# Kernel optimization log

Measured on AMD Instinct MI355X. Metric: run time of the kernel, lower is better.

Reference implementation:

```python
import jax, jax.numpy as jnp
import numpy as np

B, S, D, H, L, F = 1, 2048, 768, 12, 2, 3072
DH = D // H          # 64
W = 256              # one-sided sliding window (attention_window=512 total)
NC = S // W          # number of query chunks
VOCAB = 50265


def _ln(x, s, b, eps=1e-5):
    m = x.mean(-1, keepdims=True)
    v = ((x - m) ** 2).mean(-1, keepdims=True)
    return (x - m) / jnp.sqrt(v + eps) * s + b


def setup_inputs() -> dict:
    key = jax.random.key(0)
    ks = jax.random.split(key, 16)
    p = lambda k, sh: jax.random.normal(k, sh, jnp.float32) * 0.02
    return {
        "input_ids": jax.random.randint(ks[0], (B, S), 0, VOCAB),
        "attention_mask": jnp.ones((B, S), jnp.int32),
        "word_emb": p(ks[1], (VOCAB, D)),
        "pos_emb": p(ks[2], (S + 2, D)),          # roberta-style pos ids start at 2
        "type_emb": p(ks[3], (1, D)),
        "emb_ln_s": jnp.ones((D,), jnp.float32),
        "emb_ln_b": jnp.zeros((D,), jnp.float32),
        "Wqkv": p(ks[4], (L, 3, D, D)),
        "bqkv": jnp.zeros((L, 3, D), jnp.float32),
        "Wo": p(ks[5], (L, D, D)),
        "bo": jnp.zeros((L, D), jnp.float32),
        "ln1_s": jnp.ones((L, D), jnp.float32),
        "ln1_b": jnp.zeros((L, D), jnp.float32),
        "W1": p(ks[6], (L, D, F)),
        "b1": jnp.zeros((L, F), jnp.float32),
        "W2": p(ks[7], (L, F, D)),
        "b2": jnp.zeros((L, D), jnp.float32),
        "ln2_s": jnp.ones((L, D), jnp.float32),
        "ln2_b": jnp.zeros((L, D), jnp.float32),
        "pool_W": p(ks[8], (D, D)),
        "pool_b": jnp.zeros((D,), jnp.float32),
    }


def reference(input_ids, attention_mask, word_emb, pos_emb, type_emb,
              emb_ln_s, emb_ln_b, Wqkv, bqkv, Wo, bo, ln1_s, ln1_b,
              W1, b1, W2, b2, ln2_s, ln2_b, pool_W, pool_b):
    # ---- embeddings (roberta/longformer style) ----
    pos_ids = jnp.cumsum(attention_mask, axis=1) * attention_mask + 1  # padding_idx=1
    x = word_emb[input_ids] + pos_emb[pos_ids] + type_emb[0]
    x = _ln(x, emb_ln_s, emb_ln_b)

    # ---- banded-attention index/mask precompute (int constants) ----
    idx = jnp.arange(NC)[:, None] * W + jnp.arange(3 * W)[None, :]      # [NC, 3W] into padded seq
    rel = (jnp.arange(3 * W)[None, :] - W) - jnp.arange(W)[:, None]     # key_pos - query_pos
    band = (rel >= -W) & (rel <= W)                                      # [W, 3W]
    kmask = jnp.pad(attention_mask, ((0, 0), (W, W)))[:, idx].astype(bool)  # [B, NC, 3W]
    valid = band[None, None] & kmask[:, :, None, :]                      # [B, NC, W, 3W]

    inv_sqrt_dh = 1.0 / np.sqrt(DH)
    for l in range(L):
        qkv = jnp.einsum('bsd,tde->tbse', x, Wqkv[l]) + bqkv[l][:, None, None, :]
        q, k, v = [t.reshape(B, S, H, DH).transpose(0, 2, 1, 3) for t in qkv]  # [B,H,S,DH]
        qc = q.reshape(B, H, NC, W, DH)
        kp = jnp.pad(k, ((0, 0), (0, 0), (W, W), (0, 0)))
        vp = jnp.pad(v, ((0, 0), (0, 0), (W, W), (0, 0)))
        kc = kp[:, :, idx]                                               # [B,H,NC,3W,DH]
        vc = vp[:, :, idx]
        scores = jnp.einsum('bhcqd,bhckd->bhcqk', qc, kc) * inv_sqrt_dh  # [B,H,NC,W,3W]
        scores = jnp.where(valid[:, None], scores, -1e9)
        attn = jax.nn.softmax(scores, axis=-1)
        ctx = jnp.einsum('bhcqk,bhckd->bhcqd', attn, vc)
        ctx = ctx.reshape(B, H, S, DH).transpose(0, 2, 1, 3).reshape(B, S, D)
        x = _ln(x + ctx @ Wo[l] + bo[l], ln1_s[l], ln1_b[l])
        h = jax.nn.gelu(x @ W1[l] + b1[l], approximate=False)
        x = _ln(x + h @ W2[l] + b2[l], ln2_s[l], ln2_b[l])

    pooled = jnp.tanh(x[:, 0] @ pool_W + pool_b)
    return x, pooled
```

## Files before the change

kernel.cpp:

```cpp
#include <hip/hip_runtime.h>
#include <hip/hip_bf16.h>
#include <math.h>
#include <stddef.h>
#include <stdint.h>

typedef __hip_bfloat16 bf16;
typedef short bf16x8 __attribute__((ext_vector_type(8)));
typedef float f32x4 __attribute__((ext_vector_type(4)));

#define CS 2048
#define CD 768
#define CH 12
#define CDH 64
#define CF 3072
#define CW 256
#define CL 2
#define QKVN 2304
#define SDC ((size_t)CS * CD)
#define EPS_LD 136

__device__ __forceinline__ void gload_lds16(const bf16* g, bf16* l) {
  __builtin_amdgcn_global_load_lds(
      (const __attribute__((address_space(1))) void*)g,
      (__attribute__((address_space(3))) void*)l, 16, 0, 0);
}

__device__ __forceinline__ unsigned short f2bu(float v) {
  bf16 b = __float2bfloat16(v);
  return *(unsigned short*)&b;
}
__device__ __forceinline__ float bu2f(unsigned short u) {
  bf16 b = *(bf16*)&u;
  return __bfloat162float(b);
}

template<int NW>
__device__ __forceinline__ float block_reduce_sum(float v, float* buf) {
  #pragma unroll
  for (int off = 32; off > 0; off >>= 1) v += __shfl_down(v, off, 64);
  __syncthreads();
  if ((threadIdx.x & 63) == 0) buf[threadIdx.x >> 6] = v;
  __syncthreads();
  float s = buf[0];
  #pragma unroll
  for (int w = 1; w < NW; ++w) s += buf[w];
  return s;
}

__global__ __launch_bounds__(256) void prep_kernel(
    const float* __restrict__ Wqkv, const float* __restrict__ Wo,
    const float* __restrict__ W1, const float* __restrict__ W2,
    bf16* __restrict__ WqkvT, bf16* __restrict__ WoT,
    bf16* __restrict__ W1T, bf16* __restrict__ W2T,
    const int* __restrict__ ids, const int* __restrict__ mask,
    const float* __restrict__ wemb, const float* __restrict__ pemb,
    const float* __restrict__ temb, const float* __restrict__ gs,
    const float* __restrict__ gb, float* __restrict__ x, bf16* __restrict__ xb) {
  __shared__ float tile[64][33];
  __shared__ float red[4];
  int b = blockIdx.x;
  if (b < 6912) {
    const float* src; bf16* dst; int K, N, t;
    if (b < 1728) {
      int mat = b / 288; t = b % 288; K = 768; N = 768;
      src = Wqkv + (size_t)mat * 768 * 768; dst = WqkvT + (size_t)mat * 768 * 768;
    } else if (b < 2304) {
      b -= 1728; int mat = b / 288; t = b % 288; K = 768; N = 768;
      src = Wo + (size_t)mat * 768 * 768; dst = WoT + (size_t)mat * 768 * 768;
    } else if (b < 4608) {
      b -= 2304; int mat = b / 1152; t = b % 1152; K = 768; N = 3072;
      src = W1 + (size_t)mat * 768 * 3072; dst = W1T + (size_t)mat * 768 * 3072;
    } else {
      b -= 4608; int mat = b / 1152; t = b % 1152; K = 3072; N = 768;
      src = W2 + (size_t)mat * 3072 * 768; dst = W2T + (size_t)mat * 3072 * 768;
    }
    int nt = N / 32;
    int bn = (t % nt) * 32, bk = (t / nt) * 64;
    int tx = threadIdx.x & 31, ty = (threadIdx.x >> 5);
    #pragma unroll
    for (int i = 0; i < 8; ++i)
      tile[ty + i * 8][tx] = src[(size_t)(bk + ty + i * 8) * N + bn + tx];
    __syncthreads();
    #pragma unroll
    for (int i = 0; i < 4; ++i) {
      int n = ty + i * 8;
      if (n < 32) {
        ushort2 pk;
        pk.x = f2bu(tile[2 * tx][n]);
        pk.y = f2bu(tile[2 * tx + 1][n]);
        *(ushort2*)&dst[(size_t)(bn + n) * K + bk + 2 * tx] = pk;
      }
    }
  } else {
    int srow = b - 6912;
    int t = threadIdx.x;
    float ps = 0.f;
    for (int i = t; i <= srow; i += 256) ps += (float)mask[i];
    float tot = block_reduce_sum<4>(ps, red);
    long long pid = (long long)((int)(tot + 0.5f) * mask[srow] + 1);
    long long id = ids[srow];
    float4 v = {0.f, 0.f, 0.f, 0.f};
    if (t < 192) {
      int d = t * 4;
      float4 a = *(const float4*)&wemb[id * CD + d];
      float4 p = *(const float4*)&pemb[pid * CD + d];
      float4 tm = *(const float4*)&temb[d];
      v.x = a.x + p.x + tm.x; v.y = a.y + p.y + tm.y;
      v.z = a.z + p.z + tm.z; v.w = a.w + p.w + tm.w;
    }
    float sum = block_reduce_sum<4>(v.x + v.y + v.z + v.w, red);
    float mean = sum * (1.0f / CD);
    float cx = v.x - mean, cy = v.y - mean, cz = v.z - mean, cw = v.w - mean;
    float sqv = (t < 192) ? (cx * cx + cy * cy + cz * cz + cw * cw) : 0.f;
    float sq = block_reduce_sum<4>(sqv, red);
    float rstd = rsqrtf(sq * (1.0f / CD) + 1e-5f);
    if (t < 192) {
      int d = t * 4;
      float4 g4 = *(const float4*)&gs[d];
      float4 b4 = *(const float4*)&gb[d];
      float4 o;
      o.x = cx * rstd * g4.x + b4.x;
      o.y = cy * rstd * g4.y + b4.y;
      o.z = cz * rstd * g4.z + b4.z;
      o.w = cw * rstd * g4.w + b4.w;
      *(float4*)&x[(size_t)srow * CD + d] = o;
      ushort4 pk;
      pk.x = f2bu(o.x); pk.y = f2bu(o.y); pk.z = f2bu(o.z); pk.w = f2bu(o.w);
      *(ushort4*)&xb[(size_t)srow * CD + d] = pk;
    }
  }
}

template<int GELU, int SPLITS, int TRANS>
__device__ __forceinline__ void gemm_body(
    const bf16* __restrict__ A, const bf16* __restrict__ Bt,
    const float* __restrict__ bias, bf16* __restrict__ Cout,
    bf16* __restrict__ vTout, int M, int N, int Ktot, char* smem,
    int bx, int by) {
  bf16* As = (bf16*)smem;
  bf16* Bs = (bf16*)(smem + 64 * 64 * 2);
  bf16* eps = (bf16*)smem;
  const int tid = threadIdx.x;
  const int wave = tid >> 6, lane = tid & 63;
  const int m0 = by * 64, n0 = bx * 128;
  const int wn = wave * 64;
  const int quad = lane >> 4, rsel = lane & 15;
  const int rx = rsel & 7;
  const int r_in = lane >> 3;
  const int chunk = lane & 7;
  const int gchunk = chunk ^ r_in;
  const int Klen = Ktot / SPLITS;
  const int koff = (SPLITS > 1) ? blockIdx.z * Klen : 0;

  f32x4 acc[4][4] = {};

  for (int k0 = 0; k0 < Klen; k0 += 64) {
    #pragma unroll
    for (int i = 0; i < 12; ++i) {
      int op = wave * 12 + i;
      if (op < 8) {
        int row = op * 8 + r_in;
        gload_lds16(A + (size_t)(m0 + row) * Ktot + koff + k0 + gchunk * 8, &As[op * 512]);
      } else {
        int row = (op - 8) * 8 + r_in;
        gload_lds16(Bt + (size_t)(n0 + row) * Ktot + koff + k0 + gchunk * 8, &Bs[(op - 8) * 512]);
      }
    }
    __syncthreads();
    #pragma unroll
    for (int kh = 0; kh < 2; ++kh) {
      bf16x8 af[4], bfr[4];
      int cq = ((kh << 2) | quad);
      #pragma unroll
      for (int i = 0; i < 4; ++i)
        af[i] = *(const bf16x8*)&As[(i * 16 + rsel) * 64 + (cq ^ rx) * 8];
      #pragma unroll
      for (int j = 0; j < 4; ++j)
        bfr[j] = *(const bf16x8*)&Bs[(wn + j * 16 + rsel) * 64 + (cq ^ rx) * 8];
      #pragma unroll
      for (int i = 0; i < 4; ++i)
        #pragma unroll
        for (int j = 0; j < 4; ++j) {
          if (TRANS)
            acc[i][j] = __builtin_amdgcn_mfma_f32_16x16x32_bf16(af[i], bfr[j], acc[i][j], 0, 0, 0);
          else
            acc[i][j] = __builtin_amdgcn_mfma_f32_16x16x32_bf16(bfr[j], af[i], acc[i][j], 0, 0, 0);
        }
    }
    __syncthreads();
  }

  if (!TRANS) {
    #pragma unroll
    for (int j = 0; j < 4; ++j) {
      int cb = wn + j * 16 + quad * 4;
      float4 bv = {0.f, 0.f, 0.f, 0.f};
      if (SPLITS == 1 || blockIdx.z == 0) bv = *(const float4*)&bias[n0 + cb];
      #pragma unroll
      for (int i = 0; i < 4; ++i) {
        float v0 = acc[i][j][0] + bv.x;
        float v1 = acc[i][j][1] + bv.y;
        float v2 = acc[i][j][2] + bv.z;
        float v3 = acc[i][j][3] + bv.w;
        if (GELU) {
          v0 = 0.5f * v0 * (1.0f + erff(v0 * 0.70710678118654752f));
          v1 = 0.5f * v1 * (1.0f + erff(v1 * 0.70710678118654752f));
          v2 = 0.5f * v2 * (1.0f + erff(v2 * 0.70710678118654752f));
          v3 = 0.5f * v3 * (1.0f + erff(v3 * 0.70710678118654752f));
        }
        ushort4 pk;
        pk.x = f2bu(v0); pk.y = f2bu(v1); pk.z = f2bu(v2); pk.w = f2bu(v3);
        *(ushort4*)&eps[(i * 16 + rsel) * EPS_LD + cb] = pk;
      }
    }
    __syncthreads();
    const size_t zb = (SPLITS > 1) ? (size_t)blockIdx.z * M * N : 0;
    #pragma unroll
    for (int it = 0; it < 8; ++it) {
      int row = it * 8 + (tid >> 4);
      int c = tid & 15;
      bf16x8 v = *(const bf16x8*)&eps[row * EPS_LD + c * 8];
      *(bf16x8*)&Cout[zb + (size_t)(m0 + row) * N + n0 + c * 8] = v;
    }
  } else {
    #pragma unroll
    for (int j = 0; j < 4; ++j) {
      float bv = bias[n0 + wn + j * 16 + rsel];
      #pragma unroll
      for (int i = 0; i < 4; ++i) {
        ushort4 pk;
        pk.x = f2bu(acc[i][j][0] + bv);
        pk.y = f2bu(acc[i][j][1] + bv);
        pk.z = f2bu(acc[i][j][2] + bv);
        pk.w = f2bu(acc[i][j][3] + bv);
        *(ushort4*)&eps[(wn + j * 16 + rsel) * 72 + i * 16 + quad * 4] = pk;
      }
    }
    __syncthreads();
    #pragma unroll
    for (int it = 0; it < 8; ++it) {
      int row = it * 16 + (tid >> 3);
      int c = tid & 7;
      bf16x8 v = *(const bf16x8*)&eps[row * 72 + c * 8];
      *(bf16x8*)&vTout[(size_t)(n0 - 1536 + row) * CS + m0 + c * 8] = v;
    }
  }
}

template<int GELU, int SPLITS, int VTFUSE>
__global__ __launch_bounds__(128, 3) void gemm_mfma(
    const bf16* __restrict__ A, const bf16* __restrict__ Bt,
    const float* __restrict__ bias, bf16* __restrict__ Cout,
    bf16* __restrict__ vTout, int M, int N, int Ktot) {
  __shared__ __align__(16) char smem[24576];
  int nx = gridDim.x, ny = gridDim.y;
  int nwg = nx * ny;
  int orig = blockIdx.x + blockIdx.y * nx;
  int bx, by;
  if (nwg & 7) { bx = blockIdx.x; by = blockIdx.y; }
  else {
    int q8 = nwg >> 3;
    int nid = (orig & 7) * q8 + (orig >> 3);
    bx = nid / ny; by = nid - bx * ny;
  }
  if (VTFUSE && bx * 128 >= 1536)
    gemm_body<0, 1, 1>(A, Bt, bias, Cout, vTout, M, N, Ktot, smem, bx, by);
  else
    gemm_body<GELU, SPLITS, 0>(A, Bt, bias, Cout, vTout, M, N, Ktot, smem, bx, by);
}

__global__ __launch_bounds__(512) void attn_mfma(
    const bf16* __restrict__ qkv, const bf16* __restrict__ vT,
    const int* __restrict__ mask, bf16* __restrict__ ctx) {
  __shared__ __align__(16) bf16 Ps[8][16][72];
  __shared__ float Obuf[4][16][64];
  __shared__ float Mbuf[4][16];
  __shared__ float Lbuf[4][16];
  const int h = blockIdx.y;
  const int q0 = blockIdx.x * 64;
  const int tid = threadIdx.x;
  const int wv = tid >> 6, lane = tid & 63;
  const int qg = wv & 3, half = wv >> 2;
  const int quad = lane >> 4, rsel = lane & 15;
  const int qw = q0 + qg * 16;

  const bf16* qp = &qkv[(size_t)(qw + rsel) * QKVN + h * CDH + quad * 8];
  bf16x8 qf0 = *(const bf16x8*)qp;
  bf16x8 qf1 = *(const bf16x8*)(qp + 32);

  float mi[4], li[4];
  f32x4 o[4] = {};
  #pragma unroll
  for (int r = 0; r < 4; ++r) { mi[r] = -1e30f; li[r] = 0.f; }

  const int kt0 = half ? 5 : 0, kt1 = half ? 9 : 5;
  #pragma unroll 1
  for (int kt = kt0; kt < kt1; ++kt) {
    int kbase = qw - CW + kt * 64;
    if (kbase + 63 < 0 || kbase >= CS) continue;

    f32x4 sc[4];
    #pragma unroll
    for (int nt = 0; nt < 4; ++nt) {
      int pp = kbase + nt * 16 + rsel;
      int ppc = min(max(pp, 0), CS - 1);
      const bf16* kp = &qkv[(size_t)ppc * QKVN + 768 + h * CDH + quad * 8];
      bf16x8 kf0 = *(const bf16x8*)kp;
      bf16x8 kf1 = *(const bf16x8*)(kp + 32);
      f32x4 z = {};
      __builtin_amdgcn_s_setprio(1);
      z = __builtin_amdgcn_mfma_f32_16x16x32_bf16(qf0, kf0, z, 0, 0, 0);
      z = __builtin_amdgcn_mfma_f32_16x16x32_bf16(qf1, kf1, z, 0, 0, 0);
      __builtin_amdgcn_s_setprio(0);
      sc[nt] = z;
    }
    float mx[4] = {-1e30f, -1e30f, -1e30f, -1e30f};
    #pragma unroll
    for (int nt = 0; nt < 4; ++nt) {
      int pp = kbase + nt * 16 + rsel;
      int ppc = min(max(pp, 0), CS - 1);
      bool kvld = (pp >= 0) && (pp < CS) && (mask[ppc] != 0);
      #pragma unroll
      for (int r = 0; r < 4; ++r) {
        int qr = qw + quad * 4 + r;
        float s = sc[nt][r] * 0.125f;
        bool band = (pp >= qr - CW) && (pp <= qr + CW);
        s = (kvld && band) ? s : -1e9f;
        sc[nt][r] = s;
        mx[r] = fmaxf(mx[r], s);
      }
    }
    #pragma unroll
    for (int r = 0; r < 4; ++r) {
      #pragma unroll
      for (int off = 1; off < 16; off <<= 1)
        mx[r] = fmaxf(mx[r], __shfl_xor(mx[r], off, 64));
    }
    float al[4], rs[4] = {};
    #pragma unroll
    for (int r = 0; r < 4; ++r) {
      float mn = fmaxf(mi[r], mx[r]);
      al[r] = __expf(mi[r] - mn);
      mi[r] = mn;
    }
    #pragma unroll
    for (int nt = 0; nt < 4; ++nt)
      #pragma unroll
      for (int r = 0; r < 4; ++r) {
        float p = __expf(sc[nt][r] - mi[r]);
        sc[nt][r] = p;
        rs[r] += p;
      }
    #pragma unroll
    for (int r = 0; r < 4; ++r) {
      #pragma unroll
      for (int off = 1; off < 16; off <<= 1)
        rs[r] += __shfl_xor(rs[r], off, 64);
      li[r] = li[r] * al[r] + rs[r];
    }
    #pragma unroll
    for (int d = 0; d < 4; ++d)
      #pragma unroll
      for (int r = 0; r < 4; ++r) o[d][r] *= al[r];
    #pragma unroll
    for (int nt = 0; nt < 4; ++nt)
      #pragma unroll
      for (int r = 0; r < 4; ++r)
        Ps[wv][quad * 4 + r][nt * 16 + rsel] = __float2bfloat16(sc[nt][r]);
    __asm__ volatile("s_waitcnt lgkmcnt(0)" ::: "memory");
    bf16x8 pf0 = *(const bf16x8*)&Ps[wv][rsel][quad * 8];
    bf16x8 pf1 = *(const bf16x8*)&Ps[wv][rsel][32 + quad * 8];
    int kc0 = min(max(kbase + quad * 8, 0), CS - 8);
    int kc1 = min(max(kbase + 32 + quad * 8, 0), CS - 8);
    #pragma unroll
    for (int d = 0; d < 4; ++d) {
      const bf16* vrow = &vT[(size_t)(h * CDH + d * 16 + rsel) * CS];
      bf16x8 vf0 = *(const bf16x8*)(vrow + kc0);
      bf16x8 vf1 = *(const bf16x8*)(vrow + kc1);
      __builtin_amdgcn_s_setprio(1);
      o[d] = __builtin_amdgcn_mfma_f32_16x16x32_bf16(pf0, vf0, o[d], 0, 0, 0);
      o[d] = __builtin_amdgcn_mfma_f32_16x16x32_bf16(pf1, vf1, o[d], 0, 0, 0);
      __builtin_amdgcn_s_setprio(0);
    }
  }

  if (half == 1) {
    #pragma unroll
    for (int d = 0; d < 4; ++d)
      #pragma unroll
      for (int r = 0; r < 4; ++r)
        Obuf[qg][quad * 4 + r][d * 16 + rsel] = o[d][r];
    if (rsel == 0) {
      #pragma unroll
      for (int r = 0; r < 4; ++r) {
        Mbuf[qg][quad * 4 + r] = mi[r];
        Lbuf[qg][quad * 4 + r] = li[r];
      }
    }
  }
  __syncthreads();
  if (half == 0) {
    bf16* Cs = &Ps[qg][0][0];
    #pragma unroll
    for (int r = 0; r < 4; ++r) {
      int row = quad * 4 + r;
      float m1 = Mbuf[qg][row], l1 = Lbuf[qg][row];
      float mn = fmaxf(mi[r], m1);
      float a0 = __expf(mi[r] - mn);
      float a1 = __expf(m1 - mn);
      float inv = 1.0f / (li[r] * a0 + l1 * a1);
      #pragma unroll
      for (int d = 0; d < 4; ++d) {
        float val = (o[d][r] * a0 + Obuf[qg][row][d * 16 + rsel] * a1) * inv;
        Cs[row * 72 + d * 16 + rsel] = __float2bfloat16(val);
      }
    }
  }
  __syncthreads();
  {
    int qg2 = tid >> 7, rr = (tid >> 3) & 15, cc = tid & 7;
    bf16x8 vv = *(const bf16x8*)&Ps[qg2][rr][cc * 8];
    *(bf16x8*)&ctx[(size_t)(q0 + qg2 * 16 + rr) * CD + h * CDH + cc * 8] = vv;
  }
}

template<int P>
__global__ __launch_bounds__(192) void add_ln_kernel(
    const bf16* __restrict__ g, const float* __restrict__ xin,
    float* __restrict__ xout, bf16* __restrict__ xb,
    const float* __restrict__ gs, const float* __restrict__ gb) {
  __shared__ float red[3];
  int srow = blockIdx.x;
  int d = threadIdx.x * 4;
  size_t base = (size_t)srow * CD + d;
  float4 a = *(const float4*)&xin[base];
  #pragma unroll
  for (int p = 0; p < P; ++p) {
    ushort4 gg = *(const ushort4*)&g[p * SDC + base];
    a.x += bu2f(gg.x); a.y += bu2f(gg.y); a.z += bu2f(gg.z); a.w += bu2f(gg.w);
  }
  float sum = block_reduce_sum<3>(a.x + a.y + a.z + a.w, red);
  float mean = sum * (1.0f / CD);
  float cx = a.x - mean, cy = a.y - mean, cz = a.z - mean, cw = a.w - mean;
  float sq = block_reduce_sum<3>(cx * cx + cy * cy + cz * cz + cw * cw, red);
  float rstd = rsqrtf(sq * (1.0f / CD) + 1e-5f);
  float4 g4 = *(const float4*)&gs[d];
  float4 b4 = *(const float4*)&gb[d];
  float4 o;
  o.x = cx * rstd * g4.x + b4.x;
  o.y = cy * rstd * g4.y + b4.y;
  o.z = cz * rstd * g4.z + b4.z;
  o.w = cw * rstd * g4.w + b4.w;
  *(float4*)&xout[base] = o;
  ushort4 pk;
  pk.x = f2bu(o.x); pk.y = f2bu(o.y); pk.z = f2bu(o.z); pk.w = f2bu(o.w);
  *(ushort4*)&xb[base] = pk;
}

__global__ __launch_bounds__(256) void pool_kernel(
    const float* __restrict__ x, const float* __restrict__ Wp,
    const float* __restrict__ bp, float* __restrict__ out) {
  __shared__ float xs[CD];
  __shared__ float red[4][64];
  int t = threadIdx.x;
  for (int i = t; i < CD; i += 256) xs[i] = x[i];
  __syncthreads();
  int n = blockIdx.x * 64 + (t & 63);
  int kp = t >> 6;
  float acc = 0.f;
  #pragma unroll 4
  for (int kk = kp * 192; kk < kp * 192 + 192; ++kk)
    acc = fmaf(xs[kk], Wp[(size_t)kk * CD + n], acc);
  red[kp][t & 63] = acc;
  __syncthreads();
  if (t < 64) {
    int nn = blockIdx.x * 64 + t;
    out[nn] = tanhf(red[0][t] + red[1][t] + red[2][t] + red[3][t] + bp[nn]);
  }
}

extern "C" void kernel_launch(void* const* d_in, const int* in_sizes, int n_in,
                              void* d_out, int out_size, void* d_ws, size_t ws_size,
                              hipStream_t stream) {
  const int*   ids   = (const int*)d_in[0];
  const int*   mask  = (const int*)d_in[1];
  const float* wemb  = (const float*)d_in[2];
  const float* pemb  = (const float*)d_in[3];
  const float* temb  = (const float*)d_in[4];
  const float* elns  = (const float*)d_in[5];
  const float* elnb  = (const float*)d_in[6];
  const float* Wqkv  = (const float*)d_in[7];
  const float* bqkv  = (const float*)d_in[8];
  const float* Wo    = (const float*)d_in[9];
  const float* bo    = (const float*)d_in[10];
  const float* ln1s  = (const float*)d_in[11];
  const float* ln1b  = (const float*)d_in[12];
  const float* W1    = (const float*)d_in[13];
  const float* b1    = (const float*)d_in[14];
  const float* W2    = (const float*)d_in[15];
  const float* b2    = (const float*)d_in[16];
  const float* ln2s  = (const float*)d_in[17];
  const float* ln2b  = (const float*)d_in[18];
  const float* poolW = (const float*)d_in[19];
  const float* poolb = (const float*)d_in[20];

  const size_t SD = SDC;
  const size_t SF = (size_t)CS * CF;

  char* w = (char*)d_ws;
  float* x    = (float*)w; w += SD * 4;
  bf16*  xb   = (bf16*)w;  w += SD * 2;
  bf16*  qkv  = (bf16*)w;  w += (size_t)CS * QKVN * 2;
  bf16*  vT   = (bf16*)w;  w += SD * 2;
  bf16*  ctxb = (bf16*)w;  w += SD * 2;
  bf16*  t1b  = (bf16*)w;  w += SF * 2;
  bf16*  t2   = (bf16*)w;  w += SD * 2 * 4;
  bf16* WqkvT = (bf16*)w;  w += (size_t)CL * QKVN * CD * 2;
  bf16* WoT   = (bf16*)w;  w += (size_t)CL * CD * CD * 2;
  bf16* W1T   = (bf16*)w;  w += (size_t)CL * CF * CD * 2;
  bf16* W2T   = (bf16*)w;  w += (size_t)CL * CD * CF * 2;

  prep_kernel<<<6912 + CS, 256, 0, stream>>>(
      Wqkv, Wo, W1, W2, WqkvT, WoT, W1T, W2T,
      ids, mask, wemb, pemb, temb, elns, elnb, x, xb);

  for (int l = 0; l < CL; ++l) {
    gemm_mfma<0,1,1><<<dim3(QKVN/128, CS/64), 128, 0, stream>>>(
        xb, WqkvT + (size_t)l * QKVN * CD, bqkv + (size_t)l * 3 * CD, qkv, vT, CS, QKVN, CD);
    attn_mfma<<<dim3(CS/64, CH), 512, 0, stream>>>(qkv, vT, mask, ctxb);
    gemm_mfma<0,2,0><<<dim3(CD/128, CS/64, 2), 128, 0, stream>>>(
        ctxb, WoT + (size_t)l * CD * CD, bo + (size_t)l * CD, t2, nullptr, CS, CD, CD);
    add_ln_kernel<2><<<CS, 192, 0, stream>>>(t2, x, x, xb,
        ln1s + (size_t)l * CD, ln1b + (size_t)l * CD);
    gemm_mfma<1,1,0><<<dim3(CF/128, CS/64), 128, 0, stream>>>(
        xb, W1T + (size_t)l * CF * CD, b1 + (size_t)l * CF, t1b, nullptr, CS, CF, CD);
    gemm_mfma<0,4,0><<<dim3(CD/128, CS/64, 4), 128, 0, stream>>>(
        t1b, W2T + (size_t)l * CD * CF, b2 + (size_t)l * CD, t2, nullptr, CS, CD, CF);
    float* lastx = (l == CL - 1) ? (float*)d_out : x;
    add_ln_kernel<4><<<CS, 192, 0, stream>>>(t2, x, lastx, xb,
        ln2s + (size_t)l * CD, ln2b + (size_t)l * CD);
  }

  pool_kernel<<<12, 256, 0, stream>>>((float*)d_out, poolW, poolb, (float*)d_out + SD);
}
```

Measured before the change: 544.4 us.

## Stage shared K/V tiles in LDS for attention and halve W2 split-K

The attention kernel moves from 8 waves, which split the key range and merged their partial softmax results, to 4 waves that share one 64x64 K tile and one V tile per step. The tiles are loaded into LDS with async global-to-LDS loads and an XOR swizzle, so each tile is fetched once per block instead of once per wave from global memory. The cost is a __syncthreads per key tile and half as many waves per block. Separately, the W2 GEMM split-K drops from 4 to 2, which halves the partial-sum traffic into the following add+LN kernel but leaves fewer blocks to run in parallel.

```diff
diff --git a/kernel.cpp b/kernel.cpp
--- a/kernel.cpp
+++ b/kernel.cpp
@@ -269,20 +269,20 @@
     gemm_body<GELU, SPLITS, 0>(A, Bt, bias, Cout, vTout, M, N, Ktot, smem, bx, by);
 }
 
-__global__ __launch_bounds__(512) void attn_mfma(
+__global__ __launch_bounds__(256) void attn_mfma(
     const bf16* __restrict__ qkv, const bf16* __restrict__ vT,
     const int* __restrict__ mask, bf16* __restrict__ ctx) {
-  __shared__ __align__(16) bf16 Ps[8][16][72];
-  __shared__ float Obuf[4][16][64];
-  __shared__ float Mbuf[4][16];
-  __shared__ float Lbuf[4][16];
+  __shared__ __align__(16) bf16 Ks[64 * 64];
+  __shared__ __align__(16) bf16 Vs[64 * 64];
+  __shared__ __align__(16) bf16 Ps[4][16][72];
   const int h = blockIdx.y;
   const int q0 = blockIdx.x * 64;
   const int tid = threadIdx.x;
   const int wv = tid >> 6, lane = tid & 63;
-  const int qg = wv & 3, half = wv >> 2;
   const int quad = lane >> 4, rsel = lane & 15;
-  const int qw = q0 + qg * 16;
+  const int rx = rsel & 7;
+  const int qw = q0 + wv * 16;
+  const int r_in = lane >> 3, chunk = lane & 7, gchunk = chunk ^ r_in;
 
   const bf16* qp = &qkv[(size_t)(qw + rsel) * QKVN + h * CDH + quad * 8];
   bf16x8 qf0 = *(const bf16x8*)qp;
@@ -293,134 +293,126 @@
   #pragma unroll
   for (int r = 0; r < 4; ++r) { mi[r] = -1e30f; li[r] = 0.f; }
 
-  const int kt0 = half ? 5 : 0, kt1 = half ? 9 : 5;
   #pragma unroll 1
-  for (int kt = kt0; kt < kt1; ++kt) {
-    int kbase = qw - CW + kt * 64;
-    if (kbase + 63 < 0 || kbase >= CS) continue;
-
-    f32x4 sc[4];
-    #pragma unroll
-    for (int nt = 0; nt < 4; ++nt) {
-      int pp = kbase + nt * 16 + rsel;
-      int ppc = min(max(pp, 0), CS - 1);
-      const bf16* kp = &qkv[(size_t)ppc * QKVN + 768 + h * CDH + quad * 8];
-      bf16x8 kf0 = *(const bf16x8*)kp;
-      bf16x8 kf1 = *(const bf16x8*)(kp + 32);
-      f32x4 z = {};
-      __builtin_amdgcn_s_setprio(1);
-      z = __builtin_amdgcn_mfma_f32_16x16x32_bf16(qf0, kf0, z, 0, 0, 0);
-      z = __builtin_amdgcn_mfma_f32_16x16x32_bf16(qf1, kf1, z, 0, 0, 0);
-      __builtin_amdgcn_s_setprio(0);
-      sc[nt] = z;
-    }
-    float mx[4] = {-1e30f, -1e30f, -1e30f, -1e30f};
-    #pragma unroll
-    for (int nt = 0; nt < 4; ++nt) {
-      int pp = kbase + nt * 16 + rsel;
-      int ppc = min(max(pp, 0), CS - 1);
-      bool kvld = (pp >= 0) && (pp < CS) && (mask[ppc] != 0);
+  for (int kt = 0; kt < 9; ++kt) {
+    int kbase = q0 - CW + kt * 64;
+    bool tile_in = (kbase + 63 >= 0) && (kbase < CS);
+    if (tile_in) {
+      #pragma unroll
+      for (int i = 0; i < 4; ++i) {
+        int op = wv * 4 + i;
+        if (op < 8) {
+          int krow = min(max(kbase + op * 8 + r_in, 0), CS - 1);
+          gload_lds16(&qkv[(size_t)krow * QKVN + 768 + h * CDH + gchunk * 8], &Ks[op * 512]);
+        } else {
+          int vop = op - 8;
+          int kc = min(max(kbase + gchunk * 8, 0), CS - 8);
+          gload_lds16(&vT[(size_t)(h * CDH + vop * 8 + r_in) * CS + kc], &Vs[vop * 512]);
+        }
+      }
+    }
+    __syncthreads();
+    bool active = tile_in && (kbase + 63 >= qw - CW) && (kbase <= qw + 15 + CW);
+    if (active) {
+      f32x4 sc[4];
+      #pragma unroll
+      for (int nt = 0; nt < 4; ++nt) {
+        const bf16* kp = &Ks[(nt * 16 + rsel) * 64];
+        bf16x8 kf0 = *(const bf16x8*)(kp + (quad ^ rx) * 8);
+        bf16x8 kf1 = *(const bf16x8*)(kp + ((quad + 4) ^ rx) * 8);
+        f32x4 z = {};
+        __builtin_amdgcn_s_setprio(1);
+        z = __builtin_amdgcn_mfma_f32_16x16x32_bf16(qf0, kf0, z, 0, 0, 0);
+        z = __builtin_amdgcn_mfma_f32_16x16x32_bf16(qf1, kf1, z, 0, 0, 0);
+        __builtin_amdgcn_s_setprio(0);
+        sc[nt] = z;
+      }
+      float mx[4] = {-1e30f, -1e30f, -1e30f, -1e30f};
+      #pragma unroll
+      for (int nt = 0; nt < 4; ++nt) {
+        int pp = kbase + nt * 16 + rsel;
+        int ppc = min(max(pp, 0), CS - 1);
+        bool kvld = (pp >= 0) && (pp < CS) && (mask[ppc] != 0);
+        #pragma unroll
+        for (int r = 0; r < 4; ++r) {
+          int qr = qw + quad * 4 + r;
+          float s = sc[nt][r] * 0.125f;
+          bool band = (pp >= qr - CW) && (pp <= qr + CW);
+          s = (kvld && band) ? s : -1e9f;
+          sc[nt][r] = s;
+          mx[r] = fmaxf(mx[r], s);
+        }
+      }
       #pragma unroll
       for (int r = 0; r < 4; ++r) {
-        int qr = qw + quad * 4 + r;
-        float s = sc[nt][r] * 0.125f;
-        bool band = (pp >= qr - CW) && (pp <= qr + CW);
-        s = (kvld && band) ? s : -1e9f;
-        sc[nt][r] = s;
-        mx[r] = fmaxf(mx[r], s);
-      }
-    }
-    #pragma unroll
-    for (int r = 0; r < 4; ++r) {
-      #pragma unroll
-      for (int off = 1; off < 16; off <<= 1)
-        mx[r] = fmaxf(mx[r], __shfl_xor(mx[r], off, 64));
-    }
-    float al[4], rs[4] = {};
-    #pragma unroll
-    for (int r = 0; r < 4; ++r) {
-      float mn = fmaxf(mi[r], mx[r]);
-      al[r] = __expf(mi[r] - mn);
-      mi[r] = mn;
-    }
-    #pragma unroll
-    for (int nt = 0; nt < 4; ++nt)
+        #pragma unroll
+        for (int off = 1; off < 16; off <<= 1)
+          mx[r] = fmaxf(mx[r], __shfl_xor(mx[r], off, 64));
+      }
+      float al[4], rs[4] = {};
       #pragma unroll
       for (int r = 0; r < 4; ++r) {
-        float p = __expf(sc[nt][r] - mi[r]);
-        sc[nt][r] = p;
-        rs[r] += p;
-      }
-    #pragma unroll
-    for (int r = 0; r < 4; ++r) {
-      #pragma unroll
-      for (int off = 1; off < 16; off <<= 1)
-        rs[r] += __shfl_xor(rs[r], off, 64);
-      li[r] = li[r] * al[r] + rs[r];
-    }
-    #pragma unroll
-    for (int d = 0; d < 4; ++d)
-      #pragma unroll
-      for (int r = 0; r < 4; ++r) o[d][r] *= al[r];
-    #pragma unroll
-    for (int nt = 0; nt < 4; ++nt)
-      #pragma unroll
-      for (int r = 0; r < 4; ++r)
-        Ps[wv][quad * 4 + r][nt * 16 + rsel] = __float2bfloat16(sc[nt][r]);
-    __asm__ volatile("s_waitcnt lgkmcnt(0)" ::: "memory");
-    bf16x8 pf0 = *(const bf16x8*)&Ps[wv][rsel][quad * 8];
-    bf16x8 pf1 = *(const bf16x8*)&Ps[wv][rsel][32 + quad * 8];
-    int kc0 = min(max(kbase + quad * 8, 0), CS - 8);
-    int kc1 = min(max(kbase + 32 + quad * 8, 0), CS - 8);
-    #pragma unroll
-    for (int d = 0; d < 4; ++d) {
-      const bf16* vrow = &vT[(size_t)(h * CDH + d * 16 + rsel) * CS];
-      bf16x8 vf0 = *(const bf16x8*)(vrow + kc0);
-      bf16x8 vf1 = *(const bf16x8*)(vrow + kc1);
-      __builtin_amdgcn_s_setprio(1);
-      o[d] = __builtin_amdgcn_mfma_f32_16x16x32_bf16(pf0, vf0, o[d], 0, 0, 0);
-      o[d] = __builtin_amdgcn_mfma_f32_16x16x32_bf16(pf1, vf1, o[d], 0, 0, 0);
-      __builtin_amdgcn_s_setprio(0);
-    }
-  }
-
-  if (half == 1) {
-    #pragma unroll
-    for (int d = 0; d < 4; ++d)
-      #pragma unroll
-      for (int r = 0; r < 4; ++r)
-        Obuf[qg][quad * 4 + r][d * 16 + rsel] = o[d][r];
-    if (rsel == 0) {
+        float mn = fmaxf(mi[r], mx[r]);
+        al[r] = __expf(mi[r] - mn);
+        mi[r] = mn;
+      }
+      #pragma unroll
+      for (int nt = 0; nt < 4; ++nt)
+        #pragma unroll
+        for (int r = 0; r < 4; ++r) {
+          float p = __expf(sc[nt][r] - mi[r]);
+          sc[nt][r] = p;
+          rs[r] += p;
+        }
       #pragma unroll
       for (int r = 0; r < 4; ++r) {
-        Mbuf[qg][quad * 4 + r] = mi[r];
-        Lbuf[qg][quad * 4 + r] = li[r];
-      }
-    }
-  }
-  __syncthreads();
-  if (half == 0) {
-    bf16* Cs = &Ps[qg][0][0];
-    #pragma unroll
-    for (int r = 0; r < 4; ++r) {
-      int row = quad * 4 + r;
-      float m1 = Mbuf[qg][row], l1 = Lbuf[qg][row];
-      float mn = fmaxf(mi[r], m1);
-      float a0 = __expf(mi[r] - mn);
-      float a1 = __expf(m1 - mn);
-      float inv = 1.0f / (li[r] * a0 + l1 * a1);
+        #pragma unroll
+        for (int off = 1; off < 16; off <<= 1)
+          rs[r] += __shfl_xor(rs[r], off, 64);
+        li[r] = li[r] * al[r] + rs[r];
+      }
+      #pragma unroll
+      for (int d = 0; d < 4; ++d)
+        #pragma unroll
+        for (int r = 0; r < 4; ++r) o[d][r] *= al[r];
+      #pragma unroll
+      for (int nt = 0; nt < 4; ++nt)
+        #pragma unroll
+        for (int r = 0; r < 4; ++r)
+          Ps[wv][quad * 4 + r][nt * 16 + rsel] = __float2bfloat16(sc[nt][r]);
+      __asm__ volatile("s_waitcnt lgkmcnt(0)" ::: "memory");
+      __builtin_amdgcn_sched_barrier(0);
+      bf16x8 pf0 = *(const bf16x8*)&Ps[wv][rsel][quad * 8];
+      bf16x8 pf1 = *(const bf16x8*)&Ps[wv][rsel][32 + quad * 8];
       #pragma unroll
       for (int d = 0; d < 4; ++d) {
-        float val = (o[d][r] * a0 + Obuf[qg][row][d * 16 + rsel] * a1) * inv;
-        Cs[row * 72 + d * 16 + rsel] = __float2bfloat16(val);
-      }
-    }
-  }
-  __syncthreads();
-  {
-    int qg2 = tid >> 7, rr = (tid >> 3) & 15, cc = tid & 7;
-    bf16x8 vv = *(const bf16x8*)&Ps[qg2][rr][cc * 8];
-    *(bf16x8*)&ctx[(size_t)(q0 + qg2 * 16 + rr) * CD + h * CDH + cc * 8] = vv;
+        const bf16* vr = &Vs[(d * 16 + rsel) * 64];
+        bf16x8 vf0 = *(const bf16x8*)(vr + (quad ^ rx) * 8);
+        bf16x8 vf1 = *(const bf16x8*)(vr + ((quad + 4) ^ rx) * 8);
+        __builtin_amdgcn_s_setprio(1);
+        o[d] = __builtin_amdgcn_mfma_f32_16x16x32_bf16(pf0, vf0, o[d], 0, 0, 0);
+        o[d] = __builtin_amdgcn_mfma_f32_16x16x32_bf16(pf1, vf1, o[d], 0, 0, 0);
+        __builtin_amdgcn_s_setprio(0);
+      }
+    }
+    __syncthreads();
+  }
+
+  float inv[4];
+  #pragma unroll
+  for (int r = 0; r < 4; ++r) inv[r] = 1.0f / li[r];
+  #pragma unroll
+  for (int d = 0; d < 4; ++d)
+    #pragma unroll
+    for (int r = 0; r < 4; ++r)
+      Ps[wv][quad * 4 + r][d * 16 + rsel] = __float2bfloat16(o[d][r] * inv[r]);
+  __asm__ volatile("s_waitcnt lgkmcnt(0)" ::: "memory");
+  __builtin_amdgcn_sched_barrier(0);
+  #pragma unroll
+  for (int it = 0; it < 2; ++it) {
+    int row = it * 8 + (lane >> 3);
+    bf16x8 vv = *(const bf16x8*)&Ps[wv][row][(lane & 7) * 8];
+    *(bf16x8*)&ctx[(size_t)(qw + row) * CD + h * CDH + (lane & 7) * 8] = vv;
   }
 }
 
@@ -527,17 +519,17 @@
   for (int l = 0; l < CL; ++l) {
     gemm_mfma<0,1,1><<<dim3(QKVN/128, CS/64), 128, 0, stream>>>(
         xb, WqkvT + (size_t)l * QKVN * CD, bqkv + (size_t)l * 3 * CD, qkv, vT, CS, QKVN, CD);
-    attn_mfma<<<dim3(CS/64, CH), 512, 0, stream>>>(qkv, vT, mask, ctxb);
+    attn_mfma<<<dim3(CS/64, CH), 256, 0, stream>>>(qkv, vT, mask, ctxb);
     gemm_mfma<0,2,0><<<dim3(CD/128, CS/64, 2), 128, 0, stream>>>(
         ctxb, WoT + (size_t)l * CD * CD, bo + (size_t)l * CD, t2, nullptr, CS, CD, CD);
     add_ln_kernel<2><<<CS, 192, 0, stream>>>(t2, x, x, xb,
         ln1s + (size_t)l * CD, ln1b + (size_t)l * CD);
     gemm_mfma<1,1,0><<<dim3(CF/128, CS/64), 128, 0, stream>>>(
         xb, W1T + (size_t)l * CF * CD, b1 + (size_t)l * CF, t1b, nullptr, CS, CF, CD);
-    gemm_mfma<0,4,0><<<dim3(CD/128, CS/64, 4), 128, 0, stream>>>(
+    gemm_mfma<0,2,0><<<dim3(CD/128, CS/64, 2), 128, 0, stream>>>(
         t1b, W2T + (size_t)l * CD * CF, b2 + (size_t)l * CD, t2, nullptr, CS, CD, CF);
     float* lastx = (l == CL - 1) ? (float*)d_out : x;
-    add_ln_kernel<4><<<CS, 192, 0, stream>>>(t2, x, lastx, xb,
+    add_ln_kernel<2><<<CS, 192, 0, stream>>>(t2, x, lastx, xb,
         ln2s + (size_t)l * CD, ln2b + (size_t)l * CD);
   }
 
```

Measured after the change: 531.3 us. 2.4% less time.
